# Kernel tuning notes

Hardware: AMD Instinct MI355X
Metric: run time of the kernel (lower is better)

## Reference

```python
import jax, jax.numpy as jnp
import numpy as np

EPS = 1e-5
SLOPE = 0.2


def setup_inputs() -> dict:
    key = jax.random.key(0)
    ks = jax.random.split(key, 8)
    B, D, N = 8, 60, 1024
    dims = [(64, 120), (64, 64), (128, 64), (256, 128), (256, 512), (1024, 256)]
    inp = {"x": jax.random.normal(ks[0], (B, D, N), dtype=jnp.float32)}
    for i, (o, c) in enumerate(dims, 1):
        inp[f"w{i}"] = jax.random.normal(ks[i], (o, c), dtype=jnp.float32) / np.sqrt(c).astype(np.float32)
        inp[f"b{i}"] = jnp.zeros((o,), jnp.float32)
        inp[f"g{i}"] = jnp.ones((o,), jnp.float32)
        inp[f"be{i}"] = jnp.zeros((o,), jnp.float32)
    inp["k"] = 20
    return inp


def knn_idx(x, k):
    # x: [B, D, N] -> idx [B, N, k] of nearest neighbors (negative sq dist topk)
    inner = -2.0 * jnp.einsum('bdn,bdm->bnm', x, x)
    xx = jnp.sum(x * x, axis=1)  # [B, N]
    pd = -xx[:, :, None] - inner - xx[:, None, :]
    _, idx = jax.lax.top_k(pd, k)
    return idx


def get_graph_feature(x, k):
    # x: [B, D, N] -> [B, 2D, N, k]
    B, D, N = x.shape
    idx = knn_idx(x, k)  # [B, N, k]
    xt = jnp.transpose(x, (0, 2, 1))  # [B, N, D]
    nbr = xt[jnp.arange(B)[:, None, None], idx]  # [B, N, k, D]
    ctr = xt[:, :, None, :]  # [B, N, 1, D]
    feat = jnp.concatenate([nbr - ctr, jnp.broadcast_to(ctr, nbr.shape)], axis=-1)
    return jnp.transpose(feat, (0, 3, 1, 2))  # [B, 2D, N, k]


def lrelu(x):
    return jnp.where(x >= 0, x, SLOPE * x)


def bn(x, g, b, axes):
    # training-mode batch norm (biased variance), channel axis = 1
    m = jnp.mean(x, axis=axes, keepdims=True)
    v = jnp.mean((x - m) ** 2, axis=axes, keepdims=True)
    sh = [1] * x.ndim
    sh[1] = -1
    return (x - m) * jax.lax.rsqrt(v + EPS) * g.reshape(sh) + b.reshape(sh)


def conv2d1x1(x, w, b):
    return jnp.einsum('bcnk,oc->bonk', x, w) + b[None, :, None, None]


def conv1d1x1(x, w, b):
    return jnp.einsum('bcn,oc->bon', x, w) + b[None, :, None]


def reference(x, w1, b1, g1, be1, w2, b2, g2, be2, w3, b3, g3, be3,
              w4, b4, g4, be4, w5, b5, g5, be5, w6, b6, g6, be6, k):
    h = get_graph_feature(x, k)                             # [B,120,N,k]
    h = lrelu(bn(conv2d1x1(h, w1, b1), g1, be1, (0, 2, 3)))
    x1 = jnp.max(h, axis=-1)
    h = lrelu(bn(conv2d1x1(h, w2, b2), g2, be2, (0, 2, 3)))
    x2 = jnp.max(h, axis=-1)
    h = lrelu(bn(conv2d1x1(h, w3, b3), g3, be3, (0, 2, 3)))
    x3 = jnp.max(h, axis=-1)
    h = lrelu(bn(conv2d1x1(h, w4, b4), g4, be4, (0, 2, 3)))
    x4 = jnp.max(h, axis=-1)
    h = jnp.concatenate([x1, x2, x3, x4], axis=1)           # [B,512,N]
    h = lrelu(bn(conv1d1x1(h, w5, b5), g5, be5, (0, 2)))
    h = lrelu(bn(conv1d1x1(h, w6, b6), g6, be6, (0, 2)))
    return jnp.transpose(h, (0, 2, 1))                      # [B,N,emb_dims]
```

## Files before the change

kernel.cpp:

```cpp
#include <hip/hip_runtime.h>
#include <hip/hip_bf16.h>
#include <math.h>

#define B_ 8
#define D_ 60
#define N_ 1024
#define K_ 20
#define P1_ 8192
#define P2_ 163840

typedef __attribute__((ext_vector_type(8))) short bf16x8;
typedef __attribute__((ext_vector_type(4))) short bf16x4;
typedef __attribute__((ext_vector_type(4))) float f32x4;

__device__ inline float b2f(short s) { return __uint_as_float(((unsigned)(unsigned short)s) << 16); }
__device__ inline short f2b(float f) { __hip_bfloat16 h = __float2bfloat16(f); return *(short*)&h; }

#define OFF_IDX   0ull
#define OFF_XX    655360ull
#define OFF_STATS 688128ull
#define OFF_XT    720896ull
#define OFF_WB    1769472ull
#define OFF_XC    2662400ull
#define OFF_H5    11051008ull
#define OFF_H6    15245312ull
#define OFF_BIGA  32022528ull
#define OFF_H1    73965568ull
#define OFF_H2    94937088ull
#define OFF_H4    115908608ull
#define OFF_PART  199794688ull
#define OFF_PART2 202444800ull

#define WO1 0
#define WO2 8192
#define WO3 12288
#define WO4 20480
#define WO5 53248
#define WO6 184320

#define SO1 0
#define SO2 64
#define SO3 128
#define SO4 256
#define SO5 512
#define SO6 768
#define NCH_TOT 1792

__global__ __launch_bounds__(256) void k_xx(const float* __restrict__ x,
                                            float* __restrict__ xx) {
  int bn = blockIdx.x * 256 + threadIdx.x;
  int b = bn >> 10, n = bn & 1023;
  const float* xb = x + (size_t)b * D_ * N_ + n;
  float s = 0.f;
  for (int d = 0; d < D_; ++d) { float v = xb[(size_t)d * N_]; s += v * v; }
  xx[bn] = s;
}

__global__ __launch_bounds__(256) void k_pd(const float* __restrict__ x,
                                            const float* __restrict__ xx,
                                            float* __restrict__ pd) {
  __shared__ float lnn[D_][64];
  __shared__ float lmm[D_][128];
  int tid = threadIdx.x;
  int m0 = blockIdx.x * 128, n0 = blockIdx.y * 64, b = blockIdx.z;
  const float* xb = x + (size_t)b * D_ * N_;
  #pragma unroll
  for (int i = 0; i < 15; ++i) {
    int idx = tid + i * 256;
    int d = idx >> 6, col = idx & 63;
    lnn[d][col] = xb[(size_t)d * N_ + n0 + col];
  }
  #pragma unroll
  for (int i = 0; i < 30; ++i) {
    int idx = tid + i * 256;
    int d = idx >> 7, col = idx & 127;
    lmm[d][col] = xb[(size_t)d * N_ + m0 + col];
  }
  __syncthreads();
  int tn = tid >> 5, tm = tid & 31;
  float acc[8][4];
  #pragma unroll
  for (int i = 0; i < 8; ++i)
    #pragma unroll
    for (int j = 0; j < 4; ++j) acc[i][j] = 0.f;
  for (int d = 0; d < D_; ++d) {
    f32x4 mv  = *(const f32x4*)&lmm[d][tm * 4];
    f32x4 nva = *(const f32x4*)&lnn[d][tn * 8];
    f32x4 nvb = *(const f32x4*)&lnn[d][tn * 8 + 4];
    #pragma unroll
    for (int i = 0; i < 4; ++i)
      #pragma unroll
      for (int j = 0; j < 4; ++j) {
        acc[i][j]     = fmaf(nva[i], mv[j], acc[i][j]);
        acc[4 + i][j] = fmaf(nvb[i], mv[j], acc[4 + i][j]);
      }
  }
  const float* xxb = xx + b * 1024;
  f32x4 xxm = *(const f32x4*)(xxb + m0 + tm * 4);
  #pragma unroll
  for (int i = 0; i < 8; ++i) {
    int n = n0 + tn * 8 + i;
    float xxn = xxb[n];
    f32x4 o;
    #pragma unroll
    for (int j = 0; j < 4; ++j) o[j] = 2.f * acc[i][j] - xxn - xxm[j];
    *(f32x4*)(pd + ((size_t)(b * 1024 + n) * 1024) + m0 + tm * 4) = o;
  }
}

__global__ __launch_bounds__(256) void k_sel(const float* __restrict__ pd,
                                             int* __restrict__ idxb) {
  int tid = threadIdx.x;
  int wave = tid >> 6, lane = tid & 63;
  int bn = blockIdx.x * 4 + wave;
  const float* row = pd + (size_t)bn * 1024;
  int mbase = lane * 16;
  f32x4 r0 = *(const f32x4*)(row + mbase);
  f32x4 r1 = *(const f32x4*)(row + mbase + 4);
  f32x4 r2 = *(const f32x4*)(row + mbase + 8);
  f32x4 r3 = *(const f32x4*)(row + mbase + 12);
  float v[16];
  #pragma unroll
  for (int j = 0; j < 4; ++j) { v[j] = r0[j]; v[4 + j] = r1[j]; v[8 + j] = r2[j]; v[12 + j] = r3[j]; }
  int* outp = idxb + (size_t)bn * K_;
  for (int kk = 0; kk < K_; ++kk) {
    float bv = v[0]; int bj = 0;
    #pragma unroll
    for (int j = 1; j < 16; ++j)
      if (v[j] > bv) { bv = v[j]; bj = j; }
    int bi = mbase + bj;
    #pragma unroll
    for (int off = 1; off < 64; off <<= 1) {
      float ov = __shfl_xor(bv, off);
      int   oi = __shfl_xor(bi, off);
      if (ov > bv || (ov == bv && oi < bi)) { bv = ov; bi = oi; }
    }
    if (lane == 0) outp[kk] = bi;
    #pragma unroll
    for (int j = 0; j < 16; ++j)
      if (bi == mbase + j) v[j] = -INFINITY;
  }
}

__global__ __launch_bounds__(256) void k_xt(const float* __restrict__ x,
                                            short* __restrict__ xt) {
  int bn = blockIdx.x * 256 + threadIdx.x;
  int b = bn >> 10, n = bn & 1023;
  const float* xb = x + (size_t)b * D_ * N_ + n;
  short* row = xt + (size_t)bn * 64;
  for (int c = 0; c < 60; ++c) row[c] = f2b(xb[(size_t)c * N_]);
  row[60] = 0; row[61] = 0; row[62] = 0; row[63] = 0;
}

__global__ __launch_bounds__(256) void k_w1pad(const float* __restrict__ w1,
                                               short* __restrict__ wb) {
  int t = blockIdx.x * 256 + threadIdx.x;
  int o = t >> 7, c = t & 127;
  float v = 0.f;
  if (c < 60) v = w1[o * 120 + c];
  else if (c >= 64 && c < 124) v = w1[o * 120 + 60 + (c - 64)];
  wb[t] = f2b(v);
}

__global__ __launch_bounds__(256) void k_wcvt(const float* __restrict__ w2,
                                              const float* __restrict__ w3,
                                              const float* __restrict__ w4,
                                              const float* __restrict__ w5,
                                              const float* __restrict__ w6,
                                              short* __restrict__ wbase) {
  int t = blockIdx.x * 256 + threadIdx.x;
  if (t < 4096) wbase[WO2 + t] = f2b(w2[t]);
  else if (t < 12288) wbase[WO3 + (t - 4096)] = f2b(w3[t - 4096]);
  else if (t < 45056) wbase[WO4 + (t - 12288)] = f2b(w4[t - 12288]);
  else if (t < 176128) wbase[WO5 + (t - 45056)] = f2b(w5[t - 45056]);
  else if (t < 438272) wbase[WO6 + (t - 176128)] = f2b(w6[t - 176128]);
}

__global__ __launch_bounds__(256) void k_feat(const short* __restrict__ xt,
                                              const int* __restrict__ idxb,
                                              short* __restrict__ feat) {
  int t = blockIdx.x * 256 + threadIdx.x;
  int p = t >> 4, chunk = t & 15;
  int bn = p / K_;
  int nbr = (bn & ~1023) + idxb[p];
  bf16x8 o;
  if (chunk < 8) {
    bf16x8 c8 = *(const bf16x8*)(xt + (size_t)bn * 64 + chunk * 8);
    bf16x8 n8 = *(const bf16x8*)(xt + (size_t)nbr * 64 + chunk * 8);
    #pragma unroll
    for (int r = 0; r < 8; ++r) o[r] = f2b(b2f(n8[r]) - b2f(c8[r]));
  } else {
    o = *(const bf16x8*)(xt + (size_t)bn * 64 + (chunk - 8) * 8);
  }
  *(bf16x8*)(feat + (size_t)p * 128 + chunk * 8) = o;
}

template <int K, int COUT, bool APPLY, bool STATS>
__global__ __launch_bounds__(256) void k_gemm(const short* __restrict__ in,
                                              const short* __restrict__ wb,
                                              const float* __restrict__ bias,
                                              const float* __restrict__ Ain,
                                              const float* __restrict__ Bin,
                                              float* __restrict__ part,
                                              short* __restrict__ out) {
  constexpr int PANEL = (K < 128) ? K : 128;
  constexpr int NPAN = K / PANEL;
  constexpr int CPR = PANEL / 8;
  constexpr int CSH = (CPR == 16) ? 4 : 3;
  constexpr int PK = PANEL + 8;
  constexpr int KS = PANEL / 32;
  __shared__ short ldsA[128 * PK];
  __shared__ short ldsW[64 * PK];
  __shared__ float ls[128];
  int tid = threadIdx.x;
  int w = tid >> 6, lane = tid & 63;
  int ln = lane & 15, quad = lane >> 4;
  int co0 = blockIdx.y * 64;
  const short* srcA = in + (size_t)blockIdx.x * 128 * K;
  const short* srcW = wb + (size_t)co0 * K;

  f32x4 acc[4][2];
  #pragma unroll
  for (int m = 0; m < 4; ++m)
    #pragma unroll
    for (int t = 0; t < 2; ++t) acc[m][t] = (f32x4){0.f, 0.f, 0.f, 0.f};

  for (int pan = 0; pan < NPAN; ++pan) {
    int kp = pan * PANEL;
    if (pan) __syncthreads();
    #pragma unroll
    for (int i = 0; i < CPR / 2; ++i) {
      int g = i * 256 + tid;
      int row = g >> CSH, c = g & (CPR - 1);
      bf16x8 v = *(const bf16x8*)(srcA + (size_t)row * K + kp + c * 8);
      if (APPLY) {
        f32x4 a0 = *(const f32x4*)(Ain + kp + c * 8);
        f32x4 a1 = *(const f32x4*)(Ain + kp + c * 8 + 4);
        f32x4 b0 = *(const f32x4*)(Bin + kp + c * 8);
        f32x4 b1 = *(const f32x4*)(Bin + kp + c * 8 + 4);
        #pragma unroll
        for (int j = 0; j < 8; ++j) {
          float aj = j < 4 ? a0[j] : a1[j - 4];
          float bj = j < 4 ? b0[j] : b1[j - 4];
          float f = b2f(v[j]) * aj + bj;
          f = f >= 0.f ? f : 0.2f * f;
          v[j] = f2b(f);
        }
      }
      *(bf16x8*)(ldsA + row * PK + c * 8) = v;
    }
    #pragma unroll
    for (int i = 0; i < CPR / 4; ++i) {
      int g = i * 256 + tid;
      int row = g >> CSH, c = g & (CPR - 1);
      *(bf16x8*)(ldsW + row * PK + c * 8) =
          *(const bf16x8*)(srcW + (size_t)row * K + kp + c * 8);
    }
    __syncthreads();
    #pragma unroll
    for (int ks = 0; ks < KS; ++ks) {
      bf16x8 a[4], bfr[2];
      #pragma unroll
      for (int m = 0; m < 4; ++m)
        a[m] = *(const bf16x8*)(ldsW + (m * 16 + ln) * PK + ks * 32 + quad * 8);
      #pragma unroll
      for (int t = 0; t < 2; ++t)
        bfr[t] = *(const bf16x8*)(ldsA + (w * 32 + t * 16 + ln) * PK + ks * 32 + quad * 8);
      #pragma unroll
      for (int m = 0; m < 4; ++m)
        #pragma unroll
        for (int t = 0; t < 2; ++t)
          acc[m][t] = __builtin_amdgcn_mfma_f32_16x16x32_bf16(a[m], bfr[t], acc[m][t], 0, 0, 0);
    }
  }
  #pragma unroll
  for (int m = 0; m < 4; ++m) {
    f32x4 bs = *(const f32x4*)(bias + co0 + m * 16 + quad * 4);
    #pragma unroll
    for (int t = 0; t < 2; ++t)
      #pragma unroll
      for (int r = 0; r < 4; ++r) acc[m][t][r] += bs[r];
  }
  #pragma unroll
  for (int m = 0; m < 4; ++m)
    #pragma unroll
    for (int t = 0; t < 2; ++t) {
      int p = blockIdx.x * 128 + w * 32 + t * 16 + ln;
      bf16x4 o;
      #pragma unroll
      for (int r = 0; r < 4; ++r) o[r] = f2b(acc[m][t][r]);
      *(bf16x4*)(out + (size_t)p * COUT + co0 + m * 16 + quad * 4) = o;
    }
  if (STATS) {
    __syncthreads();
    if (tid < 128) ls[tid] = 0.f;
    __syncthreads();
    #pragma unroll
    for (int m = 0; m < 4; ++m)
      #pragma unroll
      for (int r = 0; r < 4; ++r) {
        float v0 = acc[m][0][r], v1 = acc[m][1][r];
        float s = v0 + v1, ss = v0 * v0 + v1 * v1;
        #pragma unroll
        for (int off = 1; off < 16; off <<= 1) {
          s += __shfl_xor(s, off); ss += __shfl_xor(ss, off);
        }
        if (ln == 0) {
          atomicAdd(&ls[m * 16 + quad * 4 + r], s);
          atomicAdd(&ls[64 + m * 16 + quad * 4 + r], ss);
        }
      }
    __syncthreads();
    if (tid < 128)
      part[((size_t)blockIdx.y * gridDim.x + blockIdx.x) * 128 + tid] = ls[tid];
  }
}

__global__ __launch_bounds__(256) void k_red(const float* __restrict__ part, int NB,
                                             float* __restrict__ part2) {
  int cc = blockIdx.x, by = blockIdx.y;
  int tid = threadIdx.x;
  int rg = tid >> 5;
  int c4 = (tid & 31) * 4;
  int chunk = NB >> 5;
  const float* p = part + ((size_t)cc * NB + (size_t)by * chunk) * 128;
  f32x4 acc = (f32x4){0.f, 0.f, 0.f, 0.f};
  for (int r = rg; r < chunk; r += 8) {
    f32x4 v = *(const f32x4*)(p + (size_t)r * 128 + c4);
    acc[0] += v[0]; acc[1] += v[1]; acc[2] += v[2]; acc[3] += v[3];
  }
  __shared__ float lds[1024];
  *(f32x4*)(lds + tid * 4) = acc;
  __syncthreads();
  if (tid < 32) {
    f32x4 s = (f32x4){0.f, 0.f, 0.f, 0.f};
    #pragma unroll
    for (int g = 0; g < 8; ++g) {
      f32x4 v = *(const f32x4*)(lds + (g * 32 + tid) * 4);
      s[0] += v[0]; s[1] += v[1]; s[2] += v[2]; s[3] += v[3];
    }
    *(f32x4*)(part2 + ((size_t)cc * 32 + by) * 128 + tid * 4) = s;
  }
}

__global__ __launch_bounds__(256) void k_bnab(const float* __restrict__ part, int NB,
                                              const float* __restrict__ g,
                                              const float* __restrict__ be,
                                              float* __restrict__ A,
                                              float* __restrict__ Bp, float inv) {
  __shared__ float red[256];
  int tid = threadIdx.x;
  int j = tid & 127, h = tid >> 7;
  const float* p = part + (size_t)blockIdx.x * NB * 128;
  float s = 0.f;
  for (int bx = h; bx < NB; bx += 2) s += p[(size_t)bx * 128 + j];
  red[tid] = s;
  __syncthreads();
  if (tid < 128) red[tid] = red[tid] + red[tid + 128];
  __syncthreads();
  if (tid < 64) {
    int c = blockIdx.x * 64 + tid;
    float m = red[tid] * inv;
    float v = red[64 + tid] * inv - m * m;
    float a = g[c] * rsqrtf(v + 1e-5f);
    A[c] = a; Bp[c] = be[c] - m * a;
  }
}

template <int C>
__global__ __launch_bounds__(256) void k_apply_max(const short* __restrict__ h,
                                                   const float* __restrict__ A,
                                                   const float* __restrict__ Bp,
                                                   short* __restrict__ xcat, int xoff) {
  constexpr int CH = C / 4;
  int t = blockIdx.x * 256 + threadIdx.x;
  int bn = t / CH;
  int c0 = (t % CH) * 4;
  f32x4 a = *(const f32x4*)(A + c0);
  f32x4 b = *(const f32x4*)(Bp + c0);
  float m0 = -INFINITY, m1 = -INFINITY, m2 = -INFINITY, m3 = -INFINITY;
  size_t base = (size_t)bn * K_ * C + c0;
  for (int j = 0; j < K_; ++j) {
    bf16x4 v = *(const bf16x4*)(h + base + (size_t)j * C);
    float f0 = b2f(v[0]) * a[0] + b[0]; f0 = f0 >= 0.f ? f0 : 0.2f * f0;
    float f1 = b2f(v[1]) * a[1] + b[1]; f1 = f1 >= 0.f ? f1 : 0.2f * f1;
    float f2 = b2f(v[2]) * a[2] + b[2]; f2 = f2 >= 0.f ? f2 : 0.2f * f2;
    float f3 = b2f(v[3]) * a[3] + b[3]; f3 = f3 >= 0.f ? f3 : 0.2f * f3;
    m0 = fmaxf(m0, f0); m1 = fmaxf(m1, f1); m2 = fmaxf(m2, f2); m3 = fmaxf(m3, f3);
  }
  bf16x4 o;
  o[0] = f2b(m0); o[1] = f2b(m1); o[2] = f2b(m2); o[3] = f2b(m3);
  *(bf16x4*)(xcat + (size_t)bn * 512 + xoff + c0) = o;
}

__global__ __launch_bounds__(256) void k_apply_out(const short* __restrict__ h,
                                                   const float* __restrict__ A,
                                                   const float* __restrict__ Bp,
                                                   float* __restrict__ out) {
  int t = blockIdx.x * 256 + threadIdx.x;
  int c0 = (t & 255) * 4;
  f32x4 a = *(const f32x4*)(A + c0);
  f32x4 b = *(const f32x4*)(Bp + c0);
  bf16x4 v = *(const bf16x4*)(h + (size_t)t * 4);
  f32x4 o;
  #pragma unroll
  for (int r = 0; r < 4; ++r) {
    float f = b2f(v[r]) * a[r] + b[r];
    o[r] = f >= 0.f ? f : 0.2f * f;
  }
  *(f32x4*)(out + (size_t)t * 4) = o;
}

extern "C" void kernel_launch(void* const* d_in, const int* in_sizes, int n_in,
                              void* d_out, int out_size, void* d_ws, size_t ws_size,
                              hipStream_t stream) {
  const float* x   = (const float*)d_in[0];
  const float* w1  = (const float*)d_in[1];
  const float* b1  = (const float*)d_in[2];
  const float* g1  = (const float*)d_in[3];
  const float* be1 = (const float*)d_in[4];
  const float* w2  = (const float*)d_in[5];
  const float* b2  = (const float*)d_in[6];
  const float* g2  = (const float*)d_in[7];
  const float* be2 = (const float*)d_in[8];
  const float* w3  = (const float*)d_in[9];
  const float* b3  = (const float*)d_in[10];
  const float* g3  = (const float*)d_in[11];
  const float* be3 = (const float*)d_in[12];
  const float* w4  = (const float*)d_in[13];
  const float* b4  = (const float*)d_in[14];
  const float* g4  = (const float*)d_in[15];
  const float* be4 = (const float*)d_in[16];
  const float* w5  = (const float*)d_in[17];
  const float* b5  = (const float*)d_in[18];
  const float* g5  = (const float*)d_in[19];
  const float* be5 = (const float*)d_in[20];
  const float* w6  = (const float*)d_in[21];
  const float* b6  = (const float*)d_in[22];
  const float* g6  = (const float*)d_in[23];
  const float* be6 = (const float*)d_in[24];
  float* out = (float*)d_out;
  char* ws = (char*)d_ws;

  int*   idxb = (int*)(ws + OFF_IDX);
  float* xx   = (float*)(ws + OFF_XX);
  float* Aall = (float*)(ws + OFF_STATS);
  float* Ball = Aall + NCH_TOT;
  short* xt   = (short*)(ws + OFF_XT);
  short* wbb  = (short*)(ws + OFF_WB);
  short* xcat = (short*)(ws + OFF_XC);
  short* h5   = (short*)(ws + OFF_H5);
  short* h6   = (short*)(ws + OFF_H6);
  short* feat = (short*)(ws + OFF_BIGA);
  short* h1   = (short*)(ws + OFF_H1);
  short* h2   = (short*)(ws + OFF_H2);
  short* h3   = (short*)(ws + OFF_BIGA);
  short* h4   = (short*)(ws + OFF_H4);
  float* pd    = (float*)(ws + OFF_H4);
  float* part  = (float*)(ws + OFF_PART);
  float* part2 = (float*)(ws + OFF_PART2);

  k_xx <<<P1_ / 256, 256, 0, stream>>>(x, xx);
  k_pd <<<dim3(8, 16, 8), 256, 0, stream>>>(x, xx, pd);
  k_sel<<<P1_ / 4, 256, 0, stream>>>(pd, idxb);
  k_xt <<<P1_ / 256, 256, 0, stream>>>(x, xt);
  k_w1pad<<<32, 256, 0, stream>>>(w1, wbb + WO1);
  k_wcvt<<<1712, 256, 0, stream>>>(w2, w3, w4, w5, w6, wbb);
  k_feat<<<P2_ * 16 / 256, 256, 0, stream>>>(xt, idxb, feat);

  k_gemm<128, 64, false, true><<<dim3(P2_ / 128, 1), 256, 0, stream>>>(
      feat, wbb + WO1, b1, nullptr, nullptr, part, h1);
  k_red <<<dim3(1, 32), 256, 0, stream>>>(part, P2_ / 128, part2);
  k_bnab<<<1, 256, 0, stream>>>(part2, 32, g1, be1, Aall + SO1, Ball + SO1, 1.f / P2_);
  k_apply_max<64><<<P1_ * 16 / 256, 256, 0, stream>>>(h1, Aall + SO1, Ball + SO1, xcat, 0);

  k_gemm<64, 64, true, true><<<dim3(P2_ / 128, 1), 256, 0, stream>>>(
      h1, wbb + WO2, b2, Aall + SO1, Ball + SO1, part, h2);
  k_red <<<dim3(1, 32), 256, 0, stream>>>(part, P2_ / 128, part2);
  k_bnab<<<1, 256, 0, stream>>>(part2, 32, g2, be2, Aall + SO2, Ball + SO2, 1.f / P2_);
  k_apply_max<64><<<P1_ * 16 / 256, 256, 0, stream>>>(h2, Aall + SO2, Ball + SO2, xcat, 64);

  k_gemm<64, 128, true, true><<<dim3(P2_ / 128, 2), 256, 0, stream>>>(
      h2, wbb + WO3, b3, Aall + SO2, Ball + SO2, part, h3);
  k_red <<<dim3(2, 32), 256, 0, stream>>>(part, P2_ / 128, part2);
  k_bnab<<<2, 256, 0, stream>>>(part2, 32, g3, be3, Aall + SO3, Ball + SO3, 1.f / P2_);
  k_apply_max<128><<<P1_ * 32 / 256, 256, 0, stream>>>(h3, Aall + SO3, Ball + SO3, xcat, 128);

  k_gemm<128, 256, true, true><<<dim3(P2_ / 128, 4), 256, 0, stream>>>(
      h3, wbb + WO4, b4, Aall + SO3, Ball + SO3, part, h4);
  k_red <<<dim3(4, 32), 256, 0, stream>>>(part, P2_ / 128, part2);
  k_bnab<<<4, 256, 0, stream>>>(part2, 32, g4, be4, Aall + SO4, Ball + SO4, 1.f / P2_);
  k_apply_max<256><<<P1_ * 64 / 256, 256, 0, stream>>>(h4, Aall + SO4, Ball + SO4, xcat, 256);

  k_gemm<512, 256, false, true><<<dim3(P1_ / 128, 4), 256, 0, stream>>>(
      xcat, wbb + WO5, b5, nullptr, nullptr, part, h5);
  k_bnab<<<4, 256, 0, stream>>>(part, P1_ / 128, g5, be5, Aall + SO5, Ball + SO5, 1.f / P1_);

  k_gemm<256, 1024, true, true><<<dim3(P1_ / 128, 16), 256, 0, stream>>>(
      h5, wbb + WO6, b6, Aall + SO5, Ball + SO5, part, h6);
  k_bnab<<<16, 256, 0, stream>>>(part, P1_ / 128, g6, be6, Aall + SO6, Ball + SO6, 1.f / P1_);
  k_apply_out<<<P1_ * 256 / 256, 256, 0, stream>>>(h6, Aall + SO6, Ball + SO6, out);

  (void)in_sizes; (void)n_in; (void)out_size; (void)ws_size;
}
```

Measured before the change: 442.7 us.

## Factor edge conv algebraically and fuse neighbor max into GEMM epilogues

Splits the first edge convolution into per-point neighbor and center projections, then expands them via an index gather, instead of materializing the 120-channel edge feature tensor. Max-over-neighbors is computed in the GEMM epilogue with atomicMax on order-preserving encoded floats, which removes the separate apply_max passes and the h4 store. BN and leaky-ReLU are applied to the maxima afterwards, which assumes a positive BN scale. It adds atomics, a memset, and a block-index swizzle.

```diff
diff --git a/kernel.cpp b/kernel.cpp
--- a/kernel.cpp
+++ b/kernel.cpp
@@ -15,6 +15,8 @@
 
 __device__ inline float b2f(short s) { return __uint_as_float(((unsigned)(unsigned short)s) << 16); }
 __device__ inline short f2b(float f) { __hip_bfloat16 h = __float2bfloat16(f); return *(short*)&h; }
+__device__ inline unsigned fenc(float f) { unsigned b = __float_as_uint(f); return (b & 0x80000000u) ? ~b : (b | 0x80000000u); }
+__device__ inline float fdec(unsigned k) { return __uint_as_float((k & 0x80000000u) ? (k ^ 0x80000000u) : ~k); }
 
 #define OFF_IDX   0ull
 #define OFF_XX    655360ull
@@ -24,12 +26,16 @@
 #define OFF_XC    2662400ull
 #define OFF_H5    11051008ull
 #define OFF_H6    15245312ull
-#define OFF_BIGA  32022528ull
-#define OFF_H1    73965568ull
-#define OFF_H2    94937088ull
-#define OFF_H4    115908608ull
-#define OFF_PART  199794688ull
-#define OFF_PART2 202444800ull
+#define OFF_UV    32022528ull
+#define OFF_XR1   36216832ull
+#define OFF_XR2   38313984ull
+#define OFF_XR3   40411136ull
+#define OFF_XR4   44605440ull
+#define OFF_H1    52994048ull
+#define OFF_H2    73965568ull
+#define OFF_H3    94937088ull
+#define OFF_PART  136880128ull
+#define OFF_PART2 139501568ull
 
 #define WO1 0
 #define WO2 8192
@@ -152,14 +158,17 @@
   row[60] = 0; row[61] = 0; row[62] = 0; row[63] = 0;
 }
 
-__global__ __launch_bounds__(256) void k_w1pad(const float* __restrict__ w1,
-                                               short* __restrict__ wb) {
+__global__ __launch_bounds__(256) void k_wuv(const float* __restrict__ w1,
+                                             const float* __restrict__ b1,
+                                             short* __restrict__ wuv,
+                                             float* __restrict__ buv) {
   int t = blockIdx.x * 256 + threadIdx.x;
-  int o = t >> 7, c = t & 127;
+  int o = t >> 6, c = t & 63;
   float v = 0.f;
-  if (c < 60) v = w1[o * 120 + c];
-  else if (c >= 64 && c < 124) v = w1[o * 120 + 60 + (c - 64)];
-  wb[t] = f2b(v);
+  if (o < 64) { if (c < 60) v = w1[o * 120 + c]; }
+  else { int o2 = o - 64; if (c < 60) v = w1[o2 * 120 + 60 + c] - w1[o2 * 120 + c]; }
+  wuv[t] = f2b(v);
+  if (t < 128) buv[t] = (t < 64) ? 0.f : b1[t - 64];
 }
 
 __global__ __launch_bounds__(256) void k_wcvt(const float* __restrict__ w2,
@@ -176,47 +185,39 @@
   else if (t < 438272) wbase[WO6 + (t - 176128)] = f2b(w6[t - 176128]);
 }
 
-__global__ __launch_bounds__(256) void k_feat(const short* __restrict__ xt,
-                                              const int* __restrict__ idxb,
-                                              short* __restrict__ feat) {
-  int t = blockIdx.x * 256 + threadIdx.x;
-  int p = t >> 4, chunk = t & 15;
-  int bn = p / K_;
-  int nbr = (bn & ~1023) + idxb[p];
-  bf16x8 o;
-  if (chunk < 8) {
-    bf16x8 c8 = *(const bf16x8*)(xt + (size_t)bn * 64 + chunk * 8);
-    bf16x8 n8 = *(const bf16x8*)(xt + (size_t)nbr * 64 + chunk * 8);
-    #pragma unroll
-    for (int r = 0; r < 8; ++r) o[r] = f2b(b2f(n8[r]) - b2f(c8[r]));
-  } else {
-    o = *(const bf16x8*)(xt + (size_t)bn * 64 + (chunk - 8) * 8);
-  }
-  *(bf16x8*)(feat + (size_t)p * 128 + chunk * 8) = o;
-}
-
-template <int K, int COUT, bool APPLY, bool STATS>
+template <int K, int COUT, bool APPLY, bool STATS, bool WMAX, bool HSTORE, bool F32OUT>
 __global__ __launch_bounds__(256) void k_gemm(const short* __restrict__ in,
                                               const short* __restrict__ wb,
                                               const float* __restrict__ bias,
                                               const float* __restrict__ Ain,
                                               const float* __restrict__ Bin,
                                               float* __restrict__ part,
-                                              short* __restrict__ out) {
+                                              short* __restrict__ out,
+                                              unsigned* __restrict__ umax) {
   constexpr int PANEL = (K < 128) ? K : 128;
   constexpr int NPAN = K / PANEL;
   constexpr int CPR = PANEL / 8;
   constexpr int CSH = (CPR == 16) ? 4 : 3;
   constexpr int PK = PANEL + 8;
   constexpr int KS = PANEL / 32;
-  __shared__ short ldsA[128 * PK];
-  __shared__ short ldsW[64 * PK];
-  __shared__ float ls[128];
+  constexpr int NX = COUT / 64;
+  constexpr int SA = 128 * PK * 2;
+  constexpr int SMX = WMAX ? (128 * 68 * 4) : 0;
+  constexpr int S1 = (SA > SMX) ? SA : SMX;
+  __shared__ __align__(16) char smem[S1 + 64 * PK * 2 + 512];
+  short* ldsA = (short*)smem;
+  short* ldsW = (short*)(smem + S1);
+  float* ls = (float*)(smem + S1 + 64 * PK * 2);
   int tid = threadIdx.x;
   int w = tid >> 6, lane = tid & 63;
   int ln = lane & 15, quad = lane >> 4;
-  int co0 = blockIdx.y * 64;
-  const short* srcA = in + (size_t)blockIdx.x * 128 * K;
+  int bid = blockIdx.y * NX + blockIdx.x;
+  int tot = NX * gridDim.y;
+  int gid = (bid & 7) * (tot >> 3) + (bid >> 3);
+  int bxx = gid % NX;
+  int rp = gid / NX;
+  int co0 = bxx * 64;
+  const short* srcA = in + (size_t)rp * 128 * K;
   const short* srcW = wb + (size_t)co0 * K;
 
   f32x4 acc[4][2];
@@ -281,16 +282,22 @@
       #pragma unroll
       for (int r = 0; r < 4; ++r) acc[m][t][r] += bs[r];
   }
-  #pragma unroll
-  for (int m = 0; m < 4; ++m)
-    #pragma unroll
-    for (int t = 0; t < 2; ++t) {
-      int p = blockIdx.x * 128 + w * 32 + t * 16 + ln;
-      bf16x4 o;
-      #pragma unroll
-      for (int r = 0; r < 4; ++r) o[r] = f2b(acc[m][t][r]);
-      *(bf16x4*)(out + (size_t)p * COUT + co0 + m * 16 + quad * 4) = o;
-    }
+  if (HSTORE) {
+    #pragma unroll
+    for (int m = 0; m < 4; ++m)
+      #pragma unroll
+      for (int t = 0; t < 2; ++t) {
+        int p = rp * 128 + w * 32 + t * 16 + ln;
+        if (F32OUT) {
+          *(f32x4*)((float*)out + (size_t)p * COUT + co0 + m * 16 + quad * 4) = acc[m][t];
+        } else {
+          bf16x4 o;
+          #pragma unroll
+          for (int r = 0; r < 4; ++r) o[r] = f2b(acc[m][t][r]);
+          *(bf16x4*)(out + (size_t)p * COUT + co0 + m * 16 + quad * 4) = o;
+        }
+      }
+  }
   if (STATS) {
     __syncthreads();
     if (tid < 128) ls[tid] = 0.f;
@@ -312,7 +319,82 @@
       }
     __syncthreads();
     if (tid < 128)
-      part[((size_t)blockIdx.y * gridDim.x + blockIdx.x) * 128 + tid] = ls[tid];
+      part[((size_t)bxx * gridDim.y + rp) * 128 + tid] = ls[tid];
+  }
+  if (WMAX) {
+    __syncthreads();
+    float* m32 = (float*)smem;
+    #pragma unroll
+    for (int m = 0; m < 4; ++m)
+      #pragma unroll
+      for (int t = 0; t < 2; ++t)
+        *(f32x4*)(m32 + (size_t)(w * 32 + t * 16 + ln) * 68 + m * 16 + quad * 4) = acc[m][t];
+    __syncthreads();
+    int r0 = rp * 128;
+    int pt0 = r0 / 20;
+    for (int pr = tid; pr < 512; pr += 256) {
+      int lpt = pr >> 6, col = pr & 63;
+      int ptg = pt0 + lpt;
+      int rs = ptg * 20 - r0, re = rs + 20;
+      rs = rs < 0 ? 0 : rs;
+      re = re > 128 ? 128 : re;
+      if (rs < re) {
+        float mv = -INFINITY;
+        for (int r = rs; r < re; ++r) mv = fmaxf(mv, m32[r * 68 + col]);
+        atomicMax(&umax[(size_t)ptg * COUT + co0 + col], fenc(mv));
+      }
+    }
+  }
+}
+
+__global__ __launch_bounds__(256) void k_expand(const float* __restrict__ UVf,
+                                                const int* __restrict__ idxb,
+                                                short* __restrict__ h1,
+                                                float* __restrict__ xr1,
+                                                float* __restrict__ part) {
+  int tid = threadIdx.x;
+  int lp = tid >> 4;
+  int c0 = (tid & 15) * 4;
+  int pt = blockIdx.x * 16 + lp;
+  int base = (pt >> 10) << 10;
+  f32x4 V = *(const f32x4*)(UVf + (size_t)pt * 128 + 64 + c0);
+  f32x4 sum = (f32x4){0.f, 0.f, 0.f, 0.f};
+  f32x4 ssq = (f32x4){0.f, 0.f, 0.f, 0.f};
+  f32x4 mx = (f32x4){-INFINITY, -INFINITY, -INFINITY, -INFINITY};
+  const int* ip = idxb + (size_t)pt * K_;
+  size_t hb = (size_t)pt * K_ * 64 + c0;
+  for (int k = 0; k < K_; ++k) {
+    int nb = base + ip[k];
+    f32x4 U = *(const f32x4*)(UVf + (size_t)nb * 128 + c0);
+    bf16x4 o;
+    #pragma unroll
+    for (int j = 0; j < 4; ++j) {
+      float h = U[j] + V[j];
+      mx[j] = fmaxf(mx[j], U[j]);
+      sum[j] += h; ssq[j] += h * h;
+      o[j] = f2b(h);
+    }
+    *(bf16x4*)(h1 + hb + (size_t)k * 64) = o;
+  }
+  f32x4 xo;
+  #pragma unroll
+  for (int j = 0; j < 4; ++j) xo[j] = mx[j] + V[j];
+  *(f32x4*)(xr1 + (size_t)pt * 64 + c0) = xo;
+  __shared__ float ls[2048];
+  *(f32x4*)(ls + tid * 4) = sum;
+  *(f32x4*)(ls + 1024 + tid * 4) = ssq;
+  __syncthreads();
+  if (tid < 32) {
+    int cl = tid & 15;
+    bool issq = tid >= 16;
+    const float* src = ls + (issq ? 1024 : 0);
+    f32x4 s = (f32x4){0.f, 0.f, 0.f, 0.f};
+    #pragma unroll
+    for (int g = 0; g < 16; ++g) {
+      f32x4 v = *(const f32x4*)(src + (g * 16 + cl) * 4);
+      s[0] += v[0]; s[1] += v[1]; s[2] += v[2]; s[3] += v[3];
+    }
+    *(f32x4*)(part + (size_t)blockIdx.x * 128 + (issq ? 64 : 0) + cl * 4) = s;
   }
 }
 
@@ -367,30 +449,37 @@
   }
 }
 
-template <int C>
-__global__ __launch_bounds__(256) void k_apply_max(const short* __restrict__ h,
-                                                   const float* __restrict__ A,
-                                                   const float* __restrict__ Bp,
-                                                   short* __restrict__ xcat, int xoff) {
-  constexpr int CH = C / 4;
+__global__ __launch_bounds__(256) void k_xcat(const float* __restrict__ xr1,
+                                              const unsigned* __restrict__ xr2,
+                                              const unsigned* __restrict__ xr3,
+                                              const unsigned* __restrict__ xr4,
+                                              const float* __restrict__ A,
+                                              const float* __restrict__ Bp,
+                                              short* __restrict__ xcat) {
   int t = blockIdx.x * 256 + threadIdx.x;
-  int bn = t / CH;
-  int c0 = (t % CH) * 4;
+  int p = t >> 7, cq = t & 127;
+  int c0 = cq * 4;
+  f32x4 v;
+  if (c0 < 64) {
+    v = *(const f32x4*)(xr1 + (size_t)p * 64 + c0);
+  } else {
+    const unsigned* src; int cc;
+    if (c0 < 128)      { src = xr2 + (size_t)p * 64;  cc = c0 - 64; }
+    else if (c0 < 256) { src = xr3 + (size_t)p * 128; cc = c0 - 128; }
+    else               { src = xr4 + (size_t)p * 256; cc = c0 - 256; }
+    #pragma unroll
+    for (int j = 0; j < 4; ++j) v[j] = fdec(src[cc + j]);
+  }
   f32x4 a = *(const f32x4*)(A + c0);
   f32x4 b = *(const f32x4*)(Bp + c0);
-  float m0 = -INFINITY, m1 = -INFINITY, m2 = -INFINITY, m3 = -INFINITY;
-  size_t base = (size_t)bn * K_ * C + c0;
-  for (int j = 0; j < K_; ++j) {
-    bf16x4 v = *(const bf16x4*)(h + base + (size_t)j * C);
-    float f0 = b2f(v[0]) * a[0] + b[0]; f0 = f0 >= 0.f ? f0 : 0.2f * f0;
-    float f1 = b2f(v[1]) * a[1] + b[1]; f1 = f1 >= 0.f ? f1 : 0.2f * f1;
-    float f2 = b2f(v[2]) * a[2] + b[2]; f2 = f2 >= 0.f ? f2 : 0.2f * f2;
-    float f3 = b2f(v[3]) * a[3] + b[3]; f3 = f3 >= 0.f ? f3 : 0.2f * f3;
-    m0 = fmaxf(m0, f0); m1 = fmaxf(m1, f1); m2 = fmaxf(m2, f2); m3 = fmaxf(m3, f3);
-  }
   bf16x4 o;
-  o[0] = f2b(m0); o[1] = f2b(m1); o[2] = f2b(m2); o[3] = f2b(m3);
-  *(bf16x4*)(xcat + (size_t)bn * 512 + xoff + c0) = o;
+  #pragma unroll
+  for (int j = 0; j < 4; ++j) {
+    float f = v[j] * a[j] + b[j];
+    f = f >= 0.f ? f : 0.2f * f;
+    o[j] = f2b(f);
+  }
+  *(bf16x4*)(xcat + (size_t)p * 512 + c0) = o;
 }
 
 __global__ __launch_bounds__(256) void k_apply_out(const short* __restrict__ h,
@@ -442,62 +531,66 @@
   float* out = (float*)d_out;
   char* ws = (char*)d_ws;
 
-  int*   idxb = (int*)(ws + OFF_IDX);
-  float* xx   = (float*)(ws + OFF_XX);
-  float* Aall = (float*)(ws + OFF_STATS);
-  float* Ball = Aall + NCH_TOT;
-  short* xt   = (short*)(ws + OFF_XT);
-  short* wbb  = (short*)(ws + OFF_WB);
-  short* xcat = (short*)(ws + OFF_XC);
-  short* h5   = (short*)(ws + OFF_H5);
-  short* h6   = (short*)(ws + OFF_H6);
-  short* feat = (short*)(ws + OFF_BIGA);
-  short* h1   = (short*)(ws + OFF_H1);
-  short* h2   = (short*)(ws + OFF_H2);
-  short* h3   = (short*)(ws + OFF_BIGA);
-  short* h4   = (short*)(ws + OFF_H4);
-  float* pd    = (float*)(ws + OFF_H4);
-  float* part  = (float*)(ws + OFF_PART);
-  float* part2 = (float*)(ws + OFF_PART2);
+  int*      idxb = (int*)(ws + OFF_IDX);
+  float*    xx   = (float*)(ws + OFF_XX);
+  float*    Aall = (float*)(ws + OFF_STATS);
+  float*    Ball = Aall + NCH_TOT;
+  float*    buv  = Ball + NCH_TOT;
+  short*    xt   = (short*)(ws + OFF_XT);
+  short*    wbb  = (short*)(ws + OFF_WB);
+  short*    xcat = (short*)(ws + OFF_XC);
+  short*    h5   = (short*)(ws + OFF_H5);
+  short*    h6   = (short*)(ws + OFF_H6);
+  float*    UVf  = (float*)(ws + OFF_UV);
+  float*    xr1  = (float*)(ws + OFF_XR1);
+  unsigned* xr2  = (unsigned*)(ws + OFF_XR2);
+  unsigned* xr3  = (unsigned*)(ws + OFF_XR3);
+  unsigned* xr4  = (unsigned*)(ws + OFF_XR4);
+  short*    h1   = (short*)(ws + OFF_H1);
+  short*    h2   = (short*)(ws + OFF_H2);
+  short*    h3   = (short*)(ws + OFF_H3);
+  float*    pd    = (float*)(ws + OFF_H3);
+  float*    part  = (float*)(ws + OFF_PART);
+  float*    part2 = (float*)(ws + OFF_PART2);
+
+  hipMemsetAsync(ws + OFF_XR2, 0, 2097152ull + 4194304ull + 8388608ull, stream);
 
   k_xx <<<P1_ / 256, 256, 0, stream>>>(x, xx);
   k_pd <<<dim3(8, 16, 8), 256, 0, stream>>>(x, xx, pd);
   k_sel<<<P1_ / 4, 256, 0, stream>>>(pd, idxb);
   k_xt <<<P1_ / 256, 256, 0, stream>>>(x, xt);
-  k_w1pad<<<32, 256, 0, stream>>>(w1, wbb + WO1);
+  k_wuv<<<32, 256, 0, stream>>>(w1, b1, wbb + WO1, buv);
   k_wcvt<<<1712, 256, 0, stream>>>(w2, w3, w4, w5, w6, wbb);
-  k_feat<<<P2_ * 16 / 256, 256, 0, stream>>>(xt, idxb, feat);
-
-  k_gemm<128, 64, false, true><<<dim3(P2_ / 128, 1), 256, 0, stream>>>(
-      feat, wbb + WO1, b1, nullptr, nullptr, part, h1);
-  k_red <<<dim3(1, 32), 256, 0, stream>>>(part, P2_ / 128, part2);
+
+  k_gemm<64, 128, false, false, false, true, true><<<dim3(2, 64), 256, 0, stream>>>(
+      xt, wbb + WO1, buv, nullptr, nullptr, nullptr, (short*)UVf, nullptr);
+  k_expand<<<P1_ / 16, 256, 0, stream>>>(UVf, idxb, h1, xr1, part);
+  k_red <<<dim3(1, 32), 256, 0, stream>>>(part, P1_ / 16, part2);
   k_bnab<<<1, 256, 0, stream>>>(part2, 32, g1, be1, Aall + SO1, Ball + SO1, 1.f / P2_);
-  k_apply_max<64><<<P1_ * 16 / 256, 256, 0, stream>>>(h1, Aall + SO1, Ball + SO1, xcat, 0);
-
-  k_gemm<64, 64, true, true><<<dim3(P2_ / 128, 1), 256, 0, stream>>>(
-      h1, wbb + WO2, b2, Aall + SO1, Ball + SO1, part, h2);
+
+  k_gemm<64, 64, true, true, true, true, false><<<dim3(1, P2_ / 128), 256, 0, stream>>>(
+      h1, wbb + WO2, b2, Aall + SO1, Ball + SO1, part, h2, xr2);
   k_red <<<dim3(1, 32), 256, 0, stream>>>(part, P2_ / 128, part2);
   k_bnab<<<1, 256, 0, stream>>>(part2, 32, g2, be2, Aall + SO2, Ball + SO2, 1.f / P2_);
-  k_apply_max<64><<<P1_ * 16 / 256, 256, 0, stream>>>(h2, Aall + SO2, Ball + SO2, xcat, 64);
-
-  k_gemm<64, 128, true, true><<<dim3(P2_ / 128, 2), 256, 0, stream>>>(
-      h2, wbb + WO3, b3, Aall + SO2, Ball + SO2, part, h3);
+
+  k_gemm<64, 128, true, true, true, true, false><<<dim3(2, P2_ / 128), 256, 0, stream>>>(
+      h2, wbb + WO3, b3, Aall + SO2, Ball + SO2, part, h3, xr3);
   k_red <<<dim3(2, 32), 256, 0, stream>>>(part, P2_ / 128, part2);
   k_bnab<<<2, 256, 0, stream>>>(part2, 32, g3, be3, Aall + SO3, Ball + SO3, 1.f / P2_);
-  k_apply_max<128><<<P1_ * 32 / 256, 256, 0, stream>>>(h3, Aall + SO3, Ball + SO3, xcat, 128);
-
-  k_gemm<128, 256, true, true><<<dim3(P2_ / 128, 4), 256, 0, stream>>>(
-      h3, wbb + WO4, b4, Aall + SO3, Ball + SO3, part, h4);
+
+  k_gemm<128, 256, true, true, true, false, false><<<dim3(4, P2_ / 128), 256, 0, stream>>>(
+      h3, wbb + WO4, b4, Aall + SO3, Ball + SO3, part, nullptr, xr4);
   k_red <<<dim3(4, 32), 256, 0, stream>>>(part, P2_ / 128, part2);
   k_bnab<<<4, 256, 0, stream>>>(part2, 32, g4, be4, Aall + SO4, Ball + SO4, 1.f / P2_);
-  k_apply_max<256><<<P1_ * 64 / 256, 256, 0, stream>>>(h4, Aall + SO4, Ball + SO4, xcat, 256);
-
-  k_gemm<512, 256, false, true><<<dim3(P1_ / 128, 4), 256, 0, stream>>>(
-      xcat, wbb + WO5, b5, nullptr, nullptr, part, h5);
+
+  k_xcat<<<P1_ * 128 / 256, 256, 0, stream>>>(xr1, xr2, xr3, xr4, Aall, Ball, xcat);
+
+  k_gemm<512, 256, false, true, false, true, false><<<dim3(4, P1_ / 128), 256, 0, stream>>>(
+      xcat, wbb + WO5, b5, nullptr, nullptr, part, h5, nullptr);
   k_bnab<<<4, 256, 0, stream>>>(part, P1_ / 128, g5, be5, Aall + SO5, Ball + SO5, 1.f / P1_);
 
-  k_gemm<256, 1024, true, true><<<dim3(P1_ / 128, 16), 256, 0, stream>>>(
-      h5, wbb + WO6, b6, Aall + SO5, Ball + SO5, part, h6);
+  k_gemm<256, 1024, true, true, false, true, false><<<dim3(16, P1_ / 128), 256, 0, stream>>>(
+      h5, wbb + WO6, b6, Aall + SO5, Ball + SO5, part, h6, nullptr);
   k_bnab<<<16, 256, 0, stream>>>(part, P1_ / 128, g6, be6, Aall + SO6, Ball + SO6, 1.f / P1_);
   k_apply_out<<<P1_ * 256 / 256, 256, 0, stream>>>(h6, Aall + SO6, Ball + SO6, out);
 
```

Measured after the change: 439.1 us. About the same (-0.8%).
